# Optimization experiments

Hardware: AMD Instinct MI355X
Metric: run time of the kernel (lower is better)

## Reference

```python
import jax, jax.numpy as jnp
import numpy as np

N = 6144      # nodes
IN = 512      # input_dim
D = 256       # HIDDEN_DIM (out_features per head)
H = 1         # HEADS
OUT = 128     # OUT_DIM
ALPHA = 0.2   # LeakyReLU slope
EPS = 1e-5    # LayerNorm eps


def _xavier(k, shape):
    fan_in, fan_out = shape[-2], shape[-1]
    lim = float(np.sqrt(6.0 / (fan_in + fan_out)))
    return jax.random.uniform(k, shape, jnp.float32, -lim, lim)


def _gat(x, W, a_src, a_dst, adj):
    # x: [N, IN], W: [IN, H*D], a_src/a_dst: [H, D], adj: [N, N] int
    n = x.shape[0]
    h = (x @ W).reshape(n, H, D)                       # [N, H, D]
    e1 = jnp.einsum('nhd,hd->nh', h, a_src)            # src score
    e2 = jnp.einsum('nhd,hd->nh', h, a_dst)            # dst score
    e = jax.nn.leaky_relu(e1[:, None, :] + e2[None, :, :], ALPHA)  # [N, N, H]
    e = jnp.where(adj[:, :, None] > 0, e, jnp.float32(-1e9))
    att = jnp.nan_to_num(jax.nn.softmax(e, axis=1), nan=0.0)       # softmax over dim -2 (j)
    out = jnp.einsum('nbh,bhd->nhd', att, h)           # weighted aggregation over j
    return out.reshape(n, H * D)                       # is_concat=True


def _ln(x, g, b):
    m = jnp.mean(x, axis=-1, keepdims=True)
    v = jnp.mean((x - m) ** 2, axis=-1, keepdims=True)
    return (x - m) * jax.lax.rsqrt(v + EPS) * g + b


def setup_inputs() -> dict:
    key = jax.random.key(0)
    ks = jax.random.split(key, 20)
    inp = {
        'x': jax.random.normal(ks[0], (N, IN), jnp.float32),
        'adj_cf': jax.random.randint(ks[1], (N, N), 0, 2, jnp.int32),
        'adj_org': jax.random.randint(ks[2], (N, N), 0, 2, jnp.int32),
        'adj_per': jax.random.randint(ks[3], (N, N), 0, 2, jnp.int32),
        'W_cf': _xavier(ks[4], (IN, H * D)),
        'a_src_cf': _xavier(ks[5], (H, D)),
        'a_dst_cf': _xavier(ks[6], (H, D)),
        'W_org': _xavier(ks[7], (IN, H * D)),
        'a_src_org': _xavier(ks[8], (H, D)),
        'a_dst_org': _xavier(ks[9], (H, D)),
        'W_per': _xavier(ks[10], (IN, H * D)),
        'a_src_per': _xavier(ks[11], (H, D)),
        'a_dst_per': _xavier(ks[12], (H, D)),
        'proj_W': _xavier(ks[13], (H * D, OUT)),
        'proj_b': jnp.zeros((OUT,), jnp.float32),
        'ln_g': jnp.ones((OUT,), jnp.float32),
        'ln_b': jnp.zeros((OUT,), jnp.float32),
        'alpha': jnp.ones((3, 1), jnp.float32),
    }
    return inp


def reference(x, adj_cf, adj_org, adj_per,
              W_cf, a_src_cf, a_dst_cf,
              W_org, a_src_org, a_dst_org,
              W_per, a_src_per, a_dst_per,
              proj_W, proj_b, ln_g, ln_b, alpha):
    # dropout layers are identity in eval mode
    h_cf = _gat(x, W_cf, a_src_cf, a_dst_cf, adj_cf)
    h_org = _gat(x, W_org, a_src_org, a_dst_org, adj_org)
    h_per = _gat(x, W_per, a_src_per, a_dst_per, adj_per)
    z_cf = _ln(h_cf @ proj_W + proj_b, ln_g, ln_b)
    z_org = _ln(h_org @ proj_W + proj_b, ln_g, ln_b)
    z_per = _ln(h_per @ proj_W + proj_b, ln_g, ln_b)
    w = jax.nn.softmax(alpha, axis=0)                  # [3, 1]
    z = w[0] * z_cf + w[1] * z_org + w[2] * z_per
    z = jnp.nan_to_num(z, nan=0.0, posinf=0.0, neginf=0.0)
    return (z, w)
```

## Files before the change

### kernel.cpp

```cpp
#include <hip/hip_runtime.h>

typedef _Float16 half_t;
typedef _Float16 f16x8 __attribute__((ext_vector_type(8)));
typedef _Float16 f16x4 __attribute__((ext_vector_type(4)));
typedef float f32x4 __attribute__((ext_vector_type(4)));
typedef unsigned long long u64;

#define NN 6144
#define IN_DIM 512
#define DD 256
#define OUT_DIM 128
#define SPLIT 4
#define JT 24
#define LOG2E 1.44269504088896340736f

__device__ __forceinline__ f32x4 mfma16(f16x8 a, f16x8 b, f32x4 c) {
  return __builtin_amdgcn_mfma_f32_16x16x32_f16(a, b, c, 0, 0, 0);
}

#define LBAR() asm volatile("s_waitcnt lgkmcnt(0)\n\ts_barrier" ::: "memory")
#define VWAIT(N) asm volatile("s_waitcnt vmcnt(" #N ")")
#define SBAR() __builtin_amdgcn_sched_barrier(0)

__device__ __forceinline__ unsigned enc_f(float f) {
  unsigned b = __float_as_uint(f);
  return (b & 0x80000000u) ? ~b : (b | 0x80000000u);
}
__device__ __forceinline__ float dec_f(unsigned u) {
  return (u & 0x80000000u) ? __uint_as_float(u & 0x7fffffffu)
                           : __uint_as_float(~u);
}

__global__ void cvt_kernel(const float* __restrict__ x,
                           const float* __restrict__ W0, const float* __restrict__ W1,
                           const float* __restrict__ W2, const float* __restrict__ pW,
                           half_t* __restrict__ xh, half_t* __restrict__ WT,
                           half_t* __restrict__ pWT, unsigned* __restrict__ e2mu) {
  int bx = blockIdx.x, t = threadIdx.x;
  if (bx < 3072) {
    int idx = (bx * 256 + t) * 4;
    float4 v = *(const float4*)(x + idx);
    f16x4 h;
    h[0] = (half_t)v.x; h[1] = (half_t)v.y; h[2] = (half_t)v.z; h[3] = (half_t)v.w;
    *(f16x4*)(xh + idx) = h;
    return;
  }
  int idx2 = bx - 3072;
  if (idx2 == 0 && t < 3) e2mu[t] = 0x00800000u;
  int y = idx2 >> 9;
  int idx = ((idx2 & 511) << 8) + t;
  if (y < 3) {
    const float* W = (y == 0) ? W0 : (y == 1) ? W1 : W2;
    int k = idx >> 8, n = idx & 255;
    WT[(size_t)y * DD * IN_DIM + (size_t)n * IN_DIM + k] = (half_t)W[idx];
  } else if (idx < DD * OUT_DIM) {
    int k = idx >> 7, o = idx & 127;
    pWT[(size_t)o * DD + k] = (half_t)pW[idx];
  }
}

__global__ __launch_bounds__(256, 2) void gemm1_kernel(
    const half_t* __restrict__ xh, const half_t* __restrict__ WT,
    const float* __restrict__ as0, const float* __restrict__ as1, const float* __restrict__ as2,
    const float* __restrict__ ad0, const float* __restrict__ ad1, const float* __restrict__ ad2,
    half_t* __restrict__ hT, float* __restrict__ e1,
    float* __restrict__ eb1, float* __restrict__ eb2, unsigned* __restrict__ e2mu) {
  int v = blockIdx.y;
  int i0 = blockIdx.x * 64;
  int t = threadIdx.x;
  int lane = t & 63, w = t >> 6;
  int lr = lane & 15, lg = lane >> 4;
  const half_t* Wv = WT + (size_t)v * DD * IN_DIM;
  const float* asv = (v == 0) ? as0 : (v == 1) ? as1 : as2;
  const float* adv = (v == 0) ? ad0 : (v == 1) ? ad1 : ad2;
  f32x4 acc[4][4] = {};
  for (int kt = 0; kt < 16; ++kt) {
    int k = kt * 32 + lg * 8;
    f16x8 af[4], bf[4];
#pragma unroll
    for (int mf = 0; mf < 4; ++mf)
      af[mf] = *(const f16x8*)(xh + (size_t)(i0 + mf * 16 + lr) * IN_DIM + k);
#pragma unroll
    for (int nf = 0; nf < 4; ++nf)
      bf[nf] = *(const f16x8*)(Wv + (size_t)(w * 64 + nf * 16 + lr) * IN_DIM + k);
#pragma unroll
    for (int mf = 0; mf < 4; ++mf)
#pragma unroll
      for (int nf = 0; nf < 4; ++nf)
        acc[mf][nf] = mfma16(af[mf], bf[nf], acc[mf][nf]);
  }
  __shared__ half_t tr[4][64 * 64];
  __shared__ float ep1[4][64], ep2[4][64];
  char* trw = (char*)tr[w];
#pragma unroll
  for (int mf = 0; mf < 4; ++mf)
#pragma unroll
    for (int nf = 0; nf < 4; ++nf)
#pragma unroll
      for (int r = 0; r < 4; ++r) {
        int dl = nf * 16 + lr;
        int il = mf * 16 + lg * 4 + r;
        unsigned addr = (unsigned)((dl * 128 + il * 2) ^ ((dl & 7) << 4));
        *(half_t*)(trw + addr) = (half_t)acc[mf][nf][r];
      }
  float as_c[4], ad_c[4];
#pragma unroll
  for (int nf = 0; nf < 4; ++nf) {
    int col = w * 64 + nf * 16 + lr;
    as_c[nf] = asv[col];
    ad_c[nf] = adv[col];
  }
#pragma unroll
  for (int mf = 0; mf < 4; ++mf)
#pragma unroll
    for (int r = 0; r < 4; ++r) {
      float p1 = 0.f, p2 = 0.f;
#pragma unroll
      for (int nf = 0; nf < 4; ++nf) {
        p1 = fmaf(acc[mf][nf][r], as_c[nf], p1);
        p2 = fmaf(acc[mf][nf][r], ad_c[nf], p2);
      }
      p1 += __shfl_xor(p1, 1); p1 += __shfl_xor(p1, 2);
      p1 += __shfl_xor(p1, 4); p1 += __shfl_xor(p1, 8);
      p2 += __shfl_xor(p2, 1); p2 += __shfl_xor(p2, 2);
      p2 += __shfl_xor(p2, 4); p2 += __shfl_xor(p2, 8);
      if (lr == 0) {
        int il = mf * 16 + lg * 4 + r;
        ep1[w][il] = p1;
        ep2[w][il] = p2;
      }
    }
  __syncthreads();
  half_t* hTv = hT + (size_t)v * DD * NN;
#pragma unroll
  for (int c = 0; c < 8; ++c) {
    unsigned addr = (unsigned)((lane * 128 + c * 16) ^ ((lane & 7) << 4));
    f16x8 val = *(const f16x8*)(trw + addr);
    *(f16x8*)(hTv + (size_t)(w * 64 + lane) * NN + i0 + c * 8) = val;
  }
  if (t < 64) {
    float e1v = LOG2E * (ep1[0][t] + ep1[1][t] + ep1[2][t] + ep1[3][t]);
    float e2v = LOG2E * (ep2[0][t] + ep2[1][t] + ep2[2][t] + ep2[3][t]);
    e1[v * NN + i0 + t] = e1v;
    eb1[v * NN + i0 + t] = exp2f(e2v);
    eb2[v * NN + i0 + t] = exp2f(0.2f * e2v);
    float m = e2v;
    m = fmaxf(m, __shfl_xor(m, 1));  m = fmaxf(m, __shfl_xor(m, 2));
    m = fmaxf(m, __shfl_xor(m, 4));  m = fmaxf(m, __shfl_xor(m, 8));
    m = fmaxf(m, __shfl_xor(m, 16)); m = fmaxf(m, __shfl_xor(m, 32));
    if (t == 0) atomicMax(e2mu + v, enc_f(m));
  }
}

__global__ __launch_bounds__(256, 2) void gat_kernel(
    const int* __restrict__ adj0, const int* __restrict__ adj1, const int* __restrict__ adj2,
    const half_t* __restrict__ hT,
    const float* __restrict__ e1g, const float* __restrict__ eb1g,
    const float* __restrict__ eb2g,
    const unsigned* __restrict__ e2mu, half_t* __restrict__ pacc, float* __restrict__ pl) {
  int orig = blockIdx.x;
  int swz = (orig & 7) * 144 + (orig >> 3);
  int v = swz / (96 * SPLIT);
  int rem = swz - v * (96 * SPLIT);
  int s = rem / 96;
  int i0 = (rem - s * 96) * 64;

  const int* __restrict__ adjv = (v == 0) ? adj0 : (v == 1) ? adj1 : adj2;
  int t = threadIdx.x;
  int lane = t & 63, w = t >> 6;
  int lr = lane & 15, lg = lane >> 4;
  int jq = t & 15, rg = t >> 4;

  __shared__ half_t hbuf0[DD * 64];
  __shared__ half_t hbuf1[DD * 64];
  __shared__ half_t P0[64 * 64];
  __shared__ half_t P1[64 * 64];

  const half_t* hTv = hT + (size_t)v * DD * NN;
  const float* eb1v = eb1g + v * NN;
  const float* eb2v = eb2g + v * NN;
  const int jbase = s * JT * 64;

  float A1r[4], A2r[4], thr[4];
  float e2mL = dec_f(e2mu[v]);
#pragma unroll
  for (int it = 0; it < 4; ++it) {
    float e1i = e1g[v * NN + i0 + it * 16 + rg];
    float sm = e1i + e2mL;
    float mr = fmaxf(sm, 0.2f * sm);
    A1r[it] = exp2f(e1i - mr);
    A2r[it] = exp2f(0.2f * e1i - mr);
    thr[it] = exp2f(-e1i);
  }

  f32x4 acc[4][4] = {};
  float lpart[4] = {0.f, 0.f, 0.f, 0.f};

  int sub = lane >> 3;
  int c_src = (lane & 7) ^ sub;
  auto gload = [&](half_t* hb, int jt) {
    int j0 = jbase + jt * 64;
#pragma unroll
    for (int q = 0; q < 8; ++q) {
      const half_t* gp = hTv + (size_t)(w * 64 + q * 8 + sub) * NN + j0 + c_src * 8;
      half_t* lp = hb + (w * 8 + q) * 512;
      __builtin_amdgcn_global_load_lds(
          (const __attribute__((address_space(1))) int*)gp,
          (__attribute__((address_space(3))) int*)lp, 16, 0, 0);
    }
  };
  auto load_adj = [&](int4 (&aw)[4], int jt) {
    int j0 = jbase + jt * 64;
#pragma unroll
    for (int it = 0; it < 4; ++it)
      aw[it] = *(const int4*)(adjv + (size_t)(i0 + it * 16 + rg) * NN + j0 + jq * 4);
  };
  auto comp_p = [&](const int4 (&aw)[4], const float4& b1q, const float4& b2q, char* pb) {
    float b1[4] = {b1q.x, b1q.y, b1q.z, b1q.w};
    float b2[4] = {b2q.x, b2q.y, b2q.z, b2q.w};
#pragma unroll
    for (int it = 0; it < 4; ++it) {
      int il = it * 16 + rg;
      int a4[4] = {aw[it].x, aw[it].y, aw[it].z, aw[it].w};
      f16x4 ph;
      float s0 = 0.f, s1 = 0.f;
#pragma unroll
      for (int c = 0; c < 4; ++c) {
        bool pos = b1[c] > thr[it];
        float A = pos ? A1r[it] : A2r[it];
        float B = pos ? b1[c] : b2[c];
        float p = (a4[c] > 0) ? A * B : 0.f;
        if (c & 1) s1 += p; else s0 += p;
        ph[c] = (half_t)p;
      }
      lpart[it] += s0 + s1;
      unsigned addr = (unsigned)((il * 128 + jq * 8) ^ ((il & 7) << 4));
      *(f16x4*)(pb + addr) = ph;
    }
  };
  auto do_mfma = [&](const char* pb, const half_t* hb) {
    __builtin_amdgcn_s_setprio(1);
#pragma unroll
    for (int kf = 0; kf < 2; ++kf) {
      f16x8 bfr[4];
#pragma unroll
      for (int nf = 0; nf < 4; ++nf) {
        int d = w * 64 + nf * 16 + lr;
        unsigned ba = (unsigned)(d * 128 + ((kf * 64 + lg * 16) ^ ((lr & 7) << 4)));
        bfr[nf] = *(const f16x8*)((const char*)hb + ba);
      }
#pragma unroll
      for (int mf = 0; mf < 4; ++mf) {
        int row = mf * 16 + lr;
        unsigned pa_ = (unsigned)((row * 128 + kf * 64 + lg * 16) ^ ((row & 7) << 4));
        f16x8 af = *(const f16x8*)(pb + pa_);
#pragma unroll
        for (int nf = 0; nf < 4; ++nf)
          acc[mf][nf] = mfma16(af, bfr[nf], acc[mf][nf]);
      }
    }
    __builtin_amdgcn_s_setprio(0);
  };

  int4 awA[4], awB[4];
  float4 b1A, b2A, b1B, b2B;

  load_adj(awA, 0);
  b1A = *(const float4*)(eb1v + jbase + jq * 4);
  b2A = *(const float4*)(eb2v + jbase + jq * 4);
  SBAR();
  gload(hbuf0, 0);
  SBAR();
  load_adj(awB, 1);
  b1B = *(const float4*)(eb1v + jbase + 64 + jq * 4);
  b2B = *(const float4*)(eb2v + jbase + 64 + jq * 4);
  SBAR();

#define REGION_F(T, AWc, B1c, B2c, Pc, Hc, Hn)                       \
  {                                                                  \
    comp_p(AWc, B1c, B2c, (char*)(Pc));                              \
    LBAR();                                                          \
    SBAR();                                                          \
    VWAIT(6);                                                        \
    SBAR();                                                          \
    gload(Hn, (T) + 1);                                              \
    SBAR();                                                          \
    load_adj(AWc, (T) + 2);                                          \
    B1c = *(const float4*)(eb1v + jbase + ((T) + 2) * 64 + jq * 4);  \
    B2c = *(const float4*)(eb2v + jbase + ((T) + 2) * 64 + jq * 4);  \
    SBAR();                                                          \
    do_mfma((char*)(Pc), Hc);                                        \
  }

  for (int tt = 0; tt < JT - 2; tt += 2) {
    REGION_F(tt,     awA, b1A, b2A, P0, hbuf0, hbuf1);
    REGION_F(tt + 1, awB, b1B, b2B, P1, hbuf1, hbuf0);
  }
  {
    comp_p(awA, b1A, b2A, (char*)P0);
    LBAR();
    SBAR();
    VWAIT(6);
    SBAR();
    gload(hbuf1, JT - 1);
    SBAR();
    do_mfma((char*)P0, hbuf0);
  }
  {
    comp_p(awB, b1B, b2B, (char*)P1);
    LBAR();
    SBAR();
    VWAIT(0);
    SBAR();
    do_mfma((char*)P1, hbuf1);
  }
#undef REGION_F

  size_t sl = (size_t)v * SPLIT + s;
#pragma unroll
  for (int it = 0; it < 4; ++it) {
    float ssum = lpart[it];
    ssum += __shfl_xor(ssum, 1); ssum += __shfl_xor(ssum, 2);
    ssum += __shfl_xor(ssum, 4); ssum += __shfl_xor(ssum, 8);
    if (jq == 0) pl[sl * NN + i0 + it * 16 + rg] = ssum;
  }

  half_t* pa = pacc + sl * (size_t)NN * DD;
#pragma unroll
  for (int mf = 0; mf < 4; ++mf)
#pragma unroll
    for (int r = 0; r < 4; ++r) {
      int il = mf * 16 + lg * 4 + r;
#pragma unroll
      for (int nf = 0; nf < 4; ++nf)
        pa[(size_t)(i0 + il) * DD + w * 64 + nf * 16 + lr] = (half_t)acc[mf][nf][r];
    }
}

__global__ __launch_bounds__(64) void proj_kernel(
    const half_t* __restrict__ pacc, const float* __restrict__ pl,
    const half_t* __restrict__ pWT,
    const float* __restrict__ proj_b, const float* __restrict__ ln_g,
    const float* __restrict__ ln_b, const float* __restrict__ alpha,
    float* __restrict__ out) {
  int i0 = blockIdx.x * 16;
  int t = threadIdx.x;
  int lr = t & 15, lg = t >> 4;
  float a0 = alpha[0], a1 = alpha[1], a2 = alpha[2];
  float am = fmaxf(a0, fmaxf(a1, a2));
  float x0 = __expf(a0 - am), x1 = __expf(a1 - am), x2 = __expf(a2 - am);
  float inv = 1.f / (x0 + x1 + x2);
  float wv[3] = {x0 * inv, x1 * inv, x2 * inv};
  __shared__ float rlv[3][16];
  if (t < 48) {
    int v = t >> 4, i = t & 15;
    float l = 0.f;
#pragma unroll
    for (int s = 0; s < SPLIT; ++s)
      l += pl[((size_t)v * SPLIT + s) * NN + i0 + i];
    rlv[v][i] = (l > 0.f) ? 1.f / l : 0.f;
  }
  float pb[8], gg[8], bb[8];
#pragma unroll
  for (int nf = 0; nf < 8; ++nf) {
    pb[nf] = proj_b[nf * 16 + lr];
    gg[nf] = ln_g[nf * 16 + lr];
    bb[nf] = ln_b[nf * 16 + lr];
  }
  __syncthreads();
  f32x4 zacc[8] = {};
  for (int v = 0; v < 3; ++v) {
    float rl = rlv[v][lr];
    f32x4 yac[8] = {};
    const half_t* p0 = pacc + (((size_t)v * SPLIT + 0) * NN + i0 + lr) * DD;
    const half_t* p1 = pacc + (((size_t)v * SPLIT + 1) * NN + i0 + lr) * DD;
    const half_t* p2 = pacc + (((size_t)v * SPLIT + 2) * NN + i0 + lr) * DD;
    const half_t* p3 = pacc + (((size_t)v * SPLIT + 3) * NN + i0 + lr) * DD;
    for (int kt = 0; kt < 8; ++kt) {
      int k = kt * 32 + lg * 8;
      f16x8 s0 = *(const f16x8*)(p0 + k);
      f16x8 s1 = *(const f16x8*)(p1 + k);
      f16x8 s2 = *(const f16x8*)(p2 + k);
      f16x8 s3 = *(const f16x8*)(p3 + k);
      f16x8 af;
#pragma unroll
      for (int e = 0; e < 8; ++e)
        af[e] = (half_t)((((float)s0[e] + (float)s1[e]) +
                          ((float)s2[e] + (float)s3[e])) * rl);
#pragma unroll
      for (int nf = 0; nf < 8; ++nf) {
        f16x8 bf = *(const f16x8*)(pWT + (size_t)(nf * 16 + lr) * DD + k);
        yac[nf] = mfma16(af, bf, yac[nf]);
      }
    }
#pragma unroll
    for (int r = 0; r < 4; ++r) {
      float ssum = 0.f, q = 0.f;
#pragma unroll
      for (int nf = 0; nf < 8; ++nf) {
        float y = yac[nf][r] + pb[nf];
        yac[nf][r] = y;
        ssum += y; q += y * y;
      }
      ssum += __shfl_xor(ssum, 1); ssum += __shfl_xor(ssum, 2);
      ssum += __shfl_xor(ssum, 4); ssum += __shfl_xor(ssum, 8);
      q += __shfl_xor(q, 1); q += __shfl_xor(q, 2);
      q += __shfl_xor(q, 4); q += __shfl_xor(q, 8);
      float mean = ssum * (1.f / 128.f);
      float var = q * (1.f / 128.f) - mean * mean;
      float rstd = rsqrtf(var + 1e-5f);
      float wvv = wv[v];
#pragma unroll
      for (int nf = 0; nf < 8; ++nf)
        zacc[nf][r] += wvv * (yac[nf][r] - mean) * rstd;
    }
  }
#pragma unroll
  for (int nf = 0; nf < 8; ++nf)
#pragma unroll
    for (int r = 0; r < 4; ++r) {
      int row = i0 + lg * 4 + r;
      float z = zacc[nf][r] * gg[nf] + bb[nf];
      if (!isfinite(z)) z = 0.f;
      out[(size_t)row * OUT_DIM + nf * 16 + lr] = z;
    }
  if (blockIdx.x == 0 && t < 3) out[(size_t)NN * OUT_DIM + t] = wv[t];
}

extern "C" void kernel_launch(void* const* d_in, const int* in_sizes, int n_in,
                              void* d_out, int out_size, void* d_ws, size_t ws_size,
                              hipStream_t stream) {
  const float* x      = (const float*)d_in[0];
  const int*   adj_cf = (const int*)d_in[1];
  const int*   adj_or = (const int*)d_in[2];
  const int*   adj_pe = (const int*)d_in[3];
  const float* W_cf   = (const float*)d_in[4];
  const float* as_cf  = (const float*)d_in[5];
  const float* ad_cf  = (const float*)d_in[6];
  const float* W_or   = (const float*)d_in[7];
  const float* as_or  = (const float*)d_in[8];
  const float* ad_or  = (const float*)d_in[9];
  const float* W_pe   = (const float*)d_in[10];
  const float* as_pe  = (const float*)d_in[11];
  const float* ad_pe  = (const float*)d_in[12];
  const float* proj_W = (const float*)d_in[13];
  const float* proj_b = (const float*)d_in[14];
  const float* ln_g   = (const float*)d_in[15];
  const float* ln_b   = (const float*)d_in[16];
  const float* alpha  = (const float*)d_in[17];

  char* ws = (char*)d_ws;
  half_t*   xh     = (half_t*)(ws + 0);
  half_t*   WT     = (half_t*)(ws + 6291456);
  half_t*   pWT    = (half_t*)(ws + 7077888);
  half_t*   hT     = (half_t*)(ws + 7143424);
  float*    e1     = (float*)(ws + 16580608);
  float*    eb1    = (float*)(ws + 16654336);
  float*    eb2    = (float*)(ws + 16728064);
  unsigned* e2mu   = (unsigned*)(ws + 16801792);
  half_t*   pacc   = (half_t*)(ws + 16801856);
  float*    pl     = (float*)(ws + 54550592);

  cvt_kernel<<<5120, 256, 0, stream>>>(x, W_cf, W_or, W_pe, proj_W, xh, WT, pWT, e2mu);
  gemm1_kernel<<<dim3(96, 3), 256, 0, stream>>>(xh, WT, as_cf, as_or, as_pe,
                                                ad_cf, ad_or, ad_pe, hT, e1,
                                                eb1, eb2, e2mu);
  gat_kernel<<<96 * SPLIT * 3, 256, 0, stream>>>(adj_cf, adj_or, adj_pe, hT,
                                                 e1, eb1, eb2, e2mu, pacc, pl);
  proj_kernel<<<384, 64, 0, stream>>>(pacc, pl, pWT, proj_b, ln_g, ln_b, alpha,
                                      (float*)d_out);
}
```

Baseline: 225.1 us.

## Drop LDS staging in GAT aggregation; build MFMA A-fragments in registers

The GAT aggregation kernel no longer stages h tiles and attention probabilities through shared memory with barriers. Each wave now owns 16 rows, computes its probabilities straight into an MFMA A-fragment in registers, and loads B-fragments of hT directly from global memory with 32-wide j tiles (JT doubled to keep coverage). This removes LDS traffic and block barriers. In exchange, each wave re-reads the full 256-wide hT slice from global/L2 with no reuse across waves, so global bandwidth demand rises about fourfold.

After: 703.7 us. 3.13x slower.

```diff
diff --git a/kernel.cpp b/kernel.cpp
--- a/kernel.cpp
+++ b/kernel.cpp
@@ -11,16 +11,12 @@
 #define DD 256
 #define OUT_DIM 128
 #define SPLIT 4
-#define JT 24
+#define JT 48
 #define LOG2E 1.44269504088896340736f
 
 __device__ __forceinline__ f32x4 mfma16(f16x8 a, f16x8 b, f32x4 c) {
   return __builtin_amdgcn_mfma_f32_16x16x32_f16(a, b, c, 0, 0, 0);
 }
-
-#define LBAR() asm volatile("s_waitcnt lgkmcnt(0)\n\ts_barrier" ::: "memory")
-#define VWAIT(N) asm volatile("s_waitcnt vmcnt(" #N ")")
-#define SBAR() __builtin_amdgcn_sched_barrier(0)
 
 __device__ __forceinline__ unsigned enc_f(float f) {
   unsigned b = __float_as_uint(f);
@@ -152,6 +148,12 @@
   }
 }
 
+struct TileBuf {
+  int4 a[2];
+  float4 q1[2];
+  float4 q2[2];
+};
+
 __global__ __launch_bounds__(256, 2) void gat_kernel(
     const int* __restrict__ adj0, const int* __restrict__ adj1, const int* __restrict__ adj2,
     const half_t* __restrict__ hT,
@@ -169,171 +171,92 @@
   int t = threadIdx.x;
   int lane = t & 63, w = t >> 6;
   int lr = lane & 15, lg = lane >> 4;
-  int jq = t & 15, rg = t >> 4;
-
-  __shared__ half_t hbuf0[DD * 64];
-  __shared__ half_t hbuf1[DD * 64];
-  __shared__ half_t P0[64 * 64];
-  __shared__ half_t P1[64 * 64];
+  const int jg = lg * 8;
+  const int myrow = i0 + w * 16 + lr;
 
   const half_t* hTv = hT + (size_t)v * DD * NN;
   const float* eb1v = eb1g + v * NN;
   const float* eb2v = eb2g + v * NN;
-  const int jbase = s * JT * 64;
-
-  float A1r[4], A2r[4], thr[4];
-  float e2mL = dec_f(e2mu[v]);
-#pragma unroll
-  for (int it = 0; it < 4; ++it) {
-    float e1i = e1g[v * NN + i0 + it * 16 + rg];
+  const int jbase = s * JT * 32;
+
+  float A1, A2, thr;
+  {
+    float e2mL = dec_f(e2mu[v]);
+    float e1i = e1g[v * NN + myrow];
     float sm = e1i + e2mL;
     float mr = fmaxf(sm, 0.2f * sm);
-    A1r[it] = exp2f(e1i - mr);
-    A2r[it] = exp2f(0.2f * e1i - mr);
-    thr[it] = exp2f(-e1i);
-  }
-
-  f32x4 acc[4][4] = {};
-  float lpart[4] = {0.f, 0.f, 0.f, 0.f};
-
-  int sub = lane >> 3;
-  int c_src = (lane & 7) ^ sub;
-  auto gload = [&](half_t* hb, int jt) {
-    int j0 = jbase + jt * 64;
-#pragma unroll
-    for (int q = 0; q < 8; ++q) {
-      const half_t* gp = hTv + (size_t)(w * 64 + q * 8 + sub) * NN + j0 + c_src * 8;
-      half_t* lp = hb + (w * 8 + q) * 512;
-      __builtin_amdgcn_global_load_lds(
-          (const __attribute__((address_space(1))) int*)gp,
-          (__attribute__((address_space(3))) int*)lp, 16, 0, 0);
-    }
+    A1 = exp2f(e1i - mr);
+    A2 = exp2f(0.2f * e1i - mr);
+    thr = exp2f(-e1i);
+  }
+
+  f32x4 acc[16] = {};
+  float lpart = 0.f;
+  const int* arow = adjv + (size_t)myrow * NN;
+
+  auto load_tile = [&](TileBuf& R, int jt) {
+    int j0 = jbase + jt * 32 + jg;
+    const int* ap = arow + j0;
+    R.a[0] = *(const int4*)ap;
+    R.a[1] = *(const int4*)(ap + 4);
+    R.q1[0] = *(const float4*)(eb1v + j0);
+    R.q1[1] = *(const float4*)(eb1v + j0 + 4);
+    R.q2[0] = *(const float4*)(eb2v + j0);
+    R.q2[1] = *(const float4*)(eb2v + j0 + 4);
   };
-  auto load_adj = [&](int4 (&aw)[4], int jt) {
-    int j0 = jbase + jt * 64;
-#pragma unroll
-    for (int it = 0; it < 4; ++it)
-      aw[it] = *(const int4*)(adjv + (size_t)(i0 + it * 16 + rg) * NN + j0 + jq * 4);
-  };
-  auto comp_p = [&](const int4 (&aw)[4], const float4& b1q, const float4& b2q, char* pb) {
-    float b1[4] = {b1q.x, b1q.y, b1q.z, b1q.w};
-    float b2[4] = {b2q.x, b2q.y, b2q.z, b2q.w};
-#pragma unroll
-    for (int it = 0; it < 4; ++it) {
-      int il = it * 16 + rg;
-      int a4[4] = {aw[it].x, aw[it].y, aw[it].z, aw[it].w};
-      f16x4 ph;
-      float s0 = 0.f, s1 = 0.f;
+
+  auto step = [&](const TileBuf& R, int jt) {
+    int j0 = jbase + jt * 32;
+    f16x8 af;
+    float ss = 0.f;
+#pragma unroll
+    for (int q = 0; q < 2; ++q) {
+      float b1[4] = {R.q1[q].x, R.q1[q].y, R.q1[q].z, R.q1[q].w};
+      float b2[4] = {R.q2[q].x, R.q2[q].y, R.q2[q].z, R.q2[q].w};
+      int a4[4] = {R.a[q].x, R.a[q].y, R.a[q].z, R.a[q].w};
 #pragma unroll
       for (int c = 0; c < 4; ++c) {
-        bool pos = b1[c] > thr[it];
-        float A = pos ? A1r[it] : A2r[it];
+        bool pos = b1[c] > thr;
+        float A = pos ? A1 : A2;
         float B = pos ? b1[c] : b2[c];
         float p = (a4[c] > 0) ? A * B : 0.f;
-        if (c & 1) s1 += p; else s0 += p;
-        ph[c] = (half_t)p;
-      }
-      lpart[it] += s0 + s1;
-      unsigned addr = (unsigned)((il * 128 + jq * 8) ^ ((il & 7) << 4));
-      *(f16x4*)(pb + addr) = ph;
-    }
-  };
-  auto do_mfma = [&](const char* pb, const half_t* hb) {
+        ss += p;
+        af[q * 4 + c] = (half_t)p;
+      }
+    }
+    lpart += ss;
+    const half_t* bbase = hTv + (size_t)lr * NN + j0 + jg;
     __builtin_amdgcn_s_setprio(1);
 #pragma unroll
-    for (int kf = 0; kf < 2; ++kf) {
-      f16x8 bfr[4];
-#pragma unroll
-      for (int nf = 0; nf < 4; ++nf) {
-        int d = w * 64 + nf * 16 + lr;
-        unsigned ba = (unsigned)(d * 128 + ((kf * 64 + lg * 16) ^ ((lr & 7) << 4)));
-        bfr[nf] = *(const f16x8*)((const char*)hb + ba);
-      }
-#pragma unroll
-      for (int mf = 0; mf < 4; ++mf) {
-        int row = mf * 16 + lr;
-        unsigned pa_ = (unsigned)((row * 128 + kf * 64 + lg * 16) ^ ((row & 7) << 4));
-        f16x8 af = *(const f16x8*)(pb + pa_);
-#pragma unroll
-        for (int nf = 0; nf < 4; ++nf)
-          acc[mf][nf] = mfma16(af, bfr[nf], acc[mf][nf]);
-      }
+    for (int nf = 0; nf < 16; ++nf) {
+      f16x8 bf = *(const f16x8*)(bbase + (size_t)nf * 16 * NN);
+      acc[nf] = mfma16(af, bf, acc[nf]);
     }
     __builtin_amdgcn_s_setprio(0);
   };
 
-  int4 awA[4], awB[4];
-  float4 b1A, b2A, b1B, b2B;
-
-  load_adj(awA, 0);
-  b1A = *(const float4*)(eb1v + jbase + jq * 4);
-  b2A = *(const float4*)(eb2v + jbase + jq * 4);
-  SBAR();
-  gload(hbuf0, 0);
-  SBAR();
-  load_adj(awB, 1);
-  b1B = *(const float4*)(eb1v + jbase + 64 + jq * 4);
-  b2B = *(const float4*)(eb2v + jbase + 64 + jq * 4);
-  SBAR();
-
-#define REGION_F(T, AWc, B1c, B2c, Pc, Hc, Hn)                       \
-  {                                                                  \
-    comp_p(AWc, B1c, B2c, (char*)(Pc));                              \
-    LBAR();                                                          \
-    SBAR();                                                          \
-    VWAIT(6);                                                        \
-    SBAR();                                                          \
-    gload(Hn, (T) + 1);                                              \
-    SBAR();                                                          \
-    load_adj(AWc, (T) + 2);                                          \
-    B1c = *(const float4*)(eb1v + jbase + ((T) + 2) * 64 + jq * 4);  \
-    B2c = *(const float4*)(eb2v + jbase + ((T) + 2) * 64 + jq * 4);  \
-    SBAR();                                                          \
-    do_mfma((char*)(Pc), Hc);                                        \
-  }
-
-  for (int tt = 0; tt < JT - 2; tt += 2) {
-    REGION_F(tt,     awA, b1A, b2A, P0, hbuf0, hbuf1);
-    REGION_F(tt + 1, awB, b1B, b2B, P1, hbuf1, hbuf0);
-  }
-  {
-    comp_p(awA, b1A, b2A, (char*)P0);
-    LBAR();
-    SBAR();
-    VWAIT(6);
-    SBAR();
-    gload(hbuf1, JT - 1);
-    SBAR();
-    do_mfma((char*)P0, hbuf0);
-  }
-  {
-    comp_p(awB, b1B, b2B, (char*)P1);
-    LBAR();
-    SBAR();
-    VWAIT(0);
-    SBAR();
-    do_mfma((char*)P1, hbuf1);
-  }
-#undef REGION_F
-
+  TileBuf RA, RB;
+  load_tile(RA, 0);
+  load_tile(RB, 1);
+  for (int jt = 0; jt < JT; jt += 2) {
+    step(RA, jt);
+    if (jt + 2 < JT) load_tile(RA, jt + 2);
+    step(RB, jt + 1);
+    if (jt + 3 < JT) load_tile(RB, jt + 3);
+  }
+
+  lpart += __shfl_xor(lpart, 16);
+  lpart += __shfl_xor(lpart, 32);
   size_t sl = (size_t)v * SPLIT + s;
-#pragma unroll
-  for (int it = 0; it < 4; ++it) {
-    float ssum = lpart[it];
-    ssum += __shfl_xor(ssum, 1); ssum += __shfl_xor(ssum, 2);
-    ssum += __shfl_xor(ssum, 4); ssum += __shfl_xor(ssum, 8);
-    if (jq == 0) pl[sl * NN + i0 + it * 16 + rg] = ssum;
-  }
+  if (lg == 0) pl[sl * NN + myrow] = lpart;
 
   half_t* pa = pacc + sl * (size_t)NN * DD;
 #pragma unroll
-  for (int mf = 0; mf < 4; ++mf)
+  for (int nf = 0; nf < 16; ++nf)
 #pragma unroll
     for (int r = 0; r < 4; ++r) {
-      int il = mf * 16 + lg * 4 + r;
-#pragma unroll
-      for (int nf = 0; nf < 4; ++nf)
-        pa[(size_t)(i0 + il) * DD + w * 64 + nf * 16 + lr] = (half_t)acc[mf][nf][r];
+      int row = i0 + w * 16 + lg * 4 + r;
+      pa[(size_t)row * DD + nf * 16 + lr] = (half_t)acc[nf][r];
     }
 }
 
```
